# Kernel optimization log

Hardware: AMD Instinct MI355X
Metric: run time of the kernel (lower is better)

## Reference

```python
import jax, jax.numpy as jnp
import numpy as np

B, C, D = 512, 50000, 256
N_LOADED = 40000


def setup_inputs() -> dict:
    key = jax.random.key(0)
    k1, k2, k3, k4 = jax.random.split(key, 4)
    visual_feats = jax.random.normal(k1, (B, D), dtype=jnp.float32)
    text_feats = jax.random.normal(k2, (C, D), dtype=jnp.float32)
    # sparse multi-hot labels; force class 0 positive for every row so the
    # positive set (intersected with loaded ids) is never empty
    batch_label = (jax.random.uniform(k3, (B, C)) < 0.02).astype(jnp.int32)
    batch_label = batch_label.at[:, 0].set(1)
    # distinct loaded class ids; force id 0 to be loaded
    ids = jax.random.permutation(k4, C)[:N_LOADED].astype(jnp.int32)
    ids = jnp.sort(ids).at[0].set(0)
    return {
        "visual_feats": visual_feats,
        "text_feats": text_feats,
        "batch_label": batch_label,
        "class_ids_loaded": ids,
        "d_space": D,
    }


def reference(visual_feats, text_feats, batch_label, class_ids_loaded, d_space):
    num_classes = text_feats.shape[0]
    # membership mask for loaded class ids (the set() intersection in torch)
    loaded = jnp.zeros((num_classes,), dtype=bool).at[class_ids_loaded].set(True)

    # cosine similarity; note: torch adds 1e-6 eps only to text-feature norms
    v = visual_feats / jnp.linalg.norm(visual_feats, axis=1, keepdims=True)
    t = text_feats / (1e-6 + jnp.linalg.norm(text_feats, axis=1, keepdims=True))
    S = v @ t.T  # [B, C]

    pos = (batch_label != 0) & loaded[None, :]  # ragged positive sets, as mask
    neg = (batch_label == 0) & loaded[None, :]  # ragged negative sets, as mask

    # denominator: sum of exp(sim) over negatives, per row
    denom = jnp.sum(jnp.where(neg, jnp.exp(S), 0.0), axis=1)  # [B]
    n_pos = jnp.sum(pos, axis=1).astype(S.dtype)  # [B]

    # per-row loss: mean over positives of -log(exp(s_p)/denom) = log(denom)-s_p
    per_row = jnp.sum(jnp.where(pos, jnp.log(denom)[:, None] - S, 0.0), axis=1) / n_pos
    return jnp.mean(per_row).reshape(1)
```

## Files before the change

### kernel.cpp

```cpp
#include <hip/hip_runtime.h>
#include <math.h>

#define D_DIM 256
#define GTM 64
#define GTN 64
#define BK 32
#define NB 782
#define NBP 784

typedef __attribute__((ext_vector_type(8))) short short8;
typedef __attribute__((ext_vector_type(4))) float floatx4;
typedef unsigned long long u64;

__device__ __forceinline__ unsigned short f2bf(float f) {
    unsigned int u = __float_as_uint(f);
    u += 0x7FFFu + ((u >> 16) & 1u);
    return (unsigned short)(u >> 16);
}

__device__ __forceinline__ void gload16(const void* g, void* lds) {
    __builtin_amdgcn_global_load_lds(
        (const __attribute__((address_space(1))) unsigned int*)g,
        (__attribute__((address_space(3))) unsigned int*)lds, 16, 0, 0);
}

__global__ __launch_bounds__(256) void prep(
    const float* __restrict__ V, const float* __restrict__ T,
    const int* __restrict__ ids, u64* __restrict__ loadedmask,
    unsigned short* __restrict__ Vb, unsigned short* __restrict__ Tb,
    float* __restrict__ gaccum, unsigned int* __restrict__ gcount,
    int B, int C, int n_loaded, int WPR) {
    const int tid = threadIdx.x;
    const int lane = tid & 63;
    int ptid = blockIdx.x * 256 + tid;
    if (ptid == 0) { *gcount = 0u; *gaccum = 0.f; }
    if (ptid < WPR) {
        int base = ptid << 6;
        int lo = 0, hi = n_loaded;
        while (lo < hi) { int mid = (lo + hi) >> 1; if (ids[mid] < base) lo = mid + 1; else hi = mid; }
        u64 m = 0;
        for (int i = lo; i < n_loaded; ++i) {
            int v = ids[i]; if (v >= base + 64) break;
            m |= 1ull << (v - base);
        }
        loadedmask[ptid] = m;
    }
    int pwave = blockIdx.x * 4 + (tid >> 6);
    int r0 = pwave * 4;
    if (r0 >= B + C) return;
    float4 x[4];
    #pragma unroll
    for (int q = 0; q < 4; ++q) {
        int wv = r0 + q;
        if (wv < B + C) {
            const float* src = (wv < B) ? (V + (size_t)wv * D_DIM)
                                        : (T + (size_t)(wv - B) * D_DIM);
            x[q] = ((const float4*)src)[lane];
        }
    }
    #pragma unroll
    for (int q = 0; q < 4; ++q) {
        int wv = r0 + q;
        if (wv >= B + C) break;
        bool isV = wv < B;
        float ss = x[q].x * x[q].x + x[q].y * x[q].y + x[q].z * x[q].z + x[q].w * x[q].w;
        #pragma unroll
        for (int off = 32; off > 0; off >>= 1) ss += __shfl_xor(ss, off);
        float nrm = sqrtf(ss);
        float s = isV ? (1.0f / nrm) : (1.0f / (1e-6f + nrm));
        ushort4 o;
        o.x = f2bf(x[q].x * s); o.y = f2bf(x[q].y * s);
        o.z = f2bf(x[q].z * s); o.w = f2bf(x[q].w * s);
        unsigned short* dst = isV ? (Vb + (size_t)wv * D_DIM)
                                  : (Tb + (size_t)(wv - B) * D_DIM);
        ((ushort4*)dst)[lane] = o;
    }
}

__global__ __launch_bounds__(256) void gemm_fused(
    const unsigned short* __restrict__ Vb, const unsigned short* __restrict__ Tb,
    const int* __restrict__ label, const u64* __restrict__ loadedmask,
    float* __restrict__ denomP, float* __restrict__ posP, float* __restrict__ npP,
    int C, int WPR) {
    __shared__ unsigned short As[GTM * BK];
    __shared__ unsigned short Bs[GTN * BK];
    __shared__ u64 smask[GTM];
    __shared__ float sDen[GTM], sPos[GTM], sNp[GTM];

    const int tid  = threadIdx.x;
    const int lane = tid & 63;
    const int w    = tid >> 6;
    const int m0 = blockIdx.x * GTM;
    const int n0 = blockIdx.y * GTN;

    if (tid < GTM) { sDen[tid] = 0.f; sPos[tid] = 0.f; sNp[tid] = 0.f; }

    {
        int col = n0 + lane;
        if (col >= C) col = C - 1;
        const int* lp = label + (size_t)(m0 + w * 16) * C + col;
        int labv[16];
        #pragma unroll
        for (int i = 0; i < 16; ++i) labv[i] = lp[(size_t)i * C];
        #pragma unroll
        for (int i = 0; i < 16; ++i) {
            u64 bw = __ballot(labv[i] != 0);
            if (lane == 0) smask[w * 16 + i] = bw;
        }
    }

    const int sra = lane >> 2;
    const int kc  = (lane & 3) * 8;
    int ga = m0 + w * 16 + sra;
    int gb = n0 + w * 16 + sra;
    if (gb >= C) gb = C - 1;
    const unsigned short* gA = Vb + (size_t)ga * D_DIM + kc;
    const unsigned short* gB = Tb + (size_t)gb * D_DIM + kc;
    unsigned short* lA = &As[w * 16 * BK];
    unsigned short* lB = &Bs[w * 16 * BK];

    const int wm = (w >> 1) * 32;
    const int wn = (w & 1) * 32;
    const int fr = lane & 15;
    const int quad = lane >> 4;

    floatx4 acc[2][2];
    #pragma unroll
    for (int mi = 0; mi < 2; mi++)
        #pragma unroll
        for (int ni = 0; ni < 2; ni++) acc[mi][ni] = (floatx4)0.f;

    #pragma unroll
    for (int kt = 0; kt < D_DIM / BK; ++kt) {
        if (kt) __syncthreads();
        gload16(gA + kt * BK, lA);
        gload16(gB + kt * BK, lB);
        __syncthreads();
        short8 af[2], bf[2];
        #pragma unroll
        for (int mi = 0; mi < 2; mi++)
            af[mi] = *(const short8*)&As[(wm + mi * 16 + fr) * BK + quad * 8];
        #pragma unroll
        for (int ni = 0; ni < 2; ni++)
            bf[ni] = *(const short8*)&Bs[(wn + ni * 16 + fr) * BK + quad * 8];
        #pragma unroll
        for (int mi = 0; mi < 2; mi++)
            #pragma unroll
            for (int ni = 0; ni < 2; ni++)
                acc[mi][ni] = __builtin_amdgcn_mfma_f32_16x16x32_bf16(
                    af[mi], bf[ni], acc[mi][ni], 0, 0, 0);
    }

    const u64 loadedw = loadedmask[n0 >> 6];
    #pragma unroll
    for (int mi = 0; mi < 2; mi++) {
        #pragma unroll
        for (int i = 0; i < 4; i++) {
            const int mloc = wm + mi * 16 + quad * 4 + i;
            const u64 praw = smask[mloc];
            const u64 posw = praw & loadedw;
            const u64 negw = loadedw & ~praw;
            float den = 0.f, pos = 0.f, np = 0.f;
            #pragma unroll
            for (int ni = 0; ni < 2; ni++) {
                const float s = acc[mi][ni][i];
                const int bit = wn + ni * 16 + fr;
                if ((negw >> bit) & 1) den += __expf(s);
                if ((posw >> bit) & 1) { pos += s; np += 1.f; }
            }
            #pragma unroll
            for (int off = 8; off >= 1; off >>= 1) {
                den += __shfl_xor(den, off);
                pos += __shfl_xor(pos, off);
                np  += __shfl_xor(np, off);
            }
            if (fr == 0) {
                if (den != 0.f) atomicAdd(&sDen[mloc], den);
                if (np  != 0.f) { atomicAdd(&sPos[mloc], pos); atomicAdd(&sNp[mloc], np); }
            }
        }
    }
    __syncthreads();
    if (tid < GTM) {
        denomP[(size_t)(m0 + tid) * NBP + blockIdx.y] = sDen[tid];
        posP[(size_t)(m0 + tid) * NBP + blockIdx.y]   = sPos[tid];
        npP[(size_t)(m0 + tid) * NBP + blockIdx.y]    = sNp[tid];
    }
}

__global__ void reduce_rows(const float* __restrict__ denomP, const float* __restrict__ posP,
                            const float* __restrict__ npP,
                            float* __restrict__ gaccum, unsigned int* __restrict__ gcount,
                            float* __restrict__ out, int B) {
    __shared__ float bsum[4];
    int wv   = threadIdx.x >> 6;
    int row  = blockIdx.x * 4 + wv;
    int lane = threadIdx.x & 63;
    float den = 0.f, pos = 0.f, np = 0.f;
    if (row < B) {
        for (int bn = lane; bn < NB; bn += 64) {
            den += denomP[(size_t)row * NBP + bn];
            pos += posP[(size_t)row * NBP + bn];
            np  += npP[(size_t)row * NBP + bn];
        }
        #pragma unroll
        for (int off = 32; off > 0; off >>= 1) {
            den += __shfl_xor(den, off);
            pos += __shfl_xor(pos, off);
            np  += __shfl_xor(np, off);
        }
    }
    if (lane == 0) bsum[wv] = (row < B) ? (logf(den) - pos / np) : 0.f;
    __syncthreads();
    if (threadIdx.x == 0) {
        float s = bsum[0] + bsum[1] + bsum[2] + bsum[3];
        atomicAdd(gaccum, s);
        __threadfence();
        unsigned int old = atomicAdd(gcount, 1u);
        if (old == gridDim.x - 1) {
            float tot = atomicAdd(gaccum, 0.0f);
            out[0] = tot / (float)B;
        }
    }
}

extern "C" void kernel_launch(void* const* d_in, const int* in_sizes, int n_in,
                              void* d_out, int out_size, void* d_ws, size_t ws_size,
                              hipStream_t stream) {
    const float* V     = (const float*)d_in[0];
    const float* T     = (const float*)d_in[1];
    const int*   label = (const int*)d_in[2];
    const int*   ids   = (const int*)d_in[3];
    int B = in_sizes[0] / D_DIM;
    int C = in_sizes[1] / D_DIM;
    int n_loaded = in_sizes[3];
    int WPR = (C + 63) >> 6;

    char* ws = (char*)d_ws;
    float*        gaccum = (float*)(ws + 0);
    unsigned int* gcount = (unsigned int*)(ws + 8);
    u64*   loadedmask = (u64*)(ws + 2048);
    unsigned short* Vb = (unsigned short*)(ws + 8320);
    unsigned short* Tb = (unsigned short*)(ws + 270464);
    float* denomP  = (float*)(ws + 25870464);
    float* posP    = (float*)(ws + 27476096);
    float* npP     = (float*)(ws + 29081728);

    int prep_waves  = (B + C + 3) / 4;
    int prep_blocks = (prep_waves + 3) / 4;
    prep<<<prep_blocks, 256, 0, stream>>>(
        V, T, ids, loadedmask, Vb, Tb, gaccum, gcount, B, C, n_loaded, WPR);

    dim3 grid(B / GTM, NB);
    gemm_fused<<<grid, 256, 0, stream>>>(Vb, Tb, label, loadedmask,
                                         denomP, posP, npP, C, WPR);

    reduce_rows<<<(B + 3) / 4, 256, 0, stream>>>(denomP, posP, npP,
                                                 gaccum, gcount, (float*)d_out, B);
}
```

Before: 269.0 us.

## Fuse row normalization and bf16 conversion into GEMM, vectorize label mask load

Drops the separate prep pass that normalized and bf16-converted both feature matrices. The GEMM now loads raw fp32 tiles, converts them to bf16 in registers, stores them to LDS, accumulates sum-of-squares on the fly, and applies the inverse norms to each dot product in the epilogue. This removes a full read-write of the normalized copy, but every block now reads fp32 data, twice the bytes of bf16, and redundantly recomputes norms across the 8 M-blocks and 782 N-blocks. The label mask load also switches from 16 scalar strided loads plus a ballot per row to int4 vector loads combined with shuffles.

```diff
diff --git a/kernel.cpp b/kernel.cpp
--- a/kernel.cpp
+++ b/kernel.cpp
@@ -18,24 +18,22 @@
     return (unsigned short)(u >> 16);
 }
 
-__device__ __forceinline__ void gload16(const void* g, void* lds) {
-    __builtin_amdgcn_global_load_lds(
-        (const __attribute__((address_space(1))) unsigned int*)g,
-        (__attribute__((address_space(3))) unsigned int*)lds, 16, 0, 0);
-}
-
-__global__ __launch_bounds__(256) void prep(
-    const float* __restrict__ V, const float* __restrict__ T,
-    const int* __restrict__ ids, u64* __restrict__ loadedmask,
-    unsigned short* __restrict__ Vb, unsigned short* __restrict__ Tb,
-    float* __restrict__ gaccum, unsigned int* __restrict__ gcount,
-    int B, int C, int n_loaded, int WPR) {
-    const int tid = threadIdx.x;
-    const int lane = tid & 63;
-    int ptid = blockIdx.x * 256 + tid;
-    if (ptid == 0) { *gcount = 0u; *gaccum = 0.f; }
-    if (ptid < WPR) {
-        int base = ptid << 6;
+__device__ __forceinline__ short8 pack8(float4 x, float4 y) {
+    short8 r;
+    r[0] = (short)f2bf(x.x); r[1] = (short)f2bf(x.y);
+    r[2] = (short)f2bf(x.z); r[3] = (short)f2bf(x.w);
+    r[4] = (short)f2bf(y.x); r[5] = (short)f2bf(y.y);
+    r[6] = (short)f2bf(y.z); r[7] = (short)f2bf(y.w);
+    return r;
+}
+
+__global__ void prep_mask(const int* __restrict__ ids, u64* __restrict__ loadedmask,
+                          float* __restrict__ gaccum, unsigned int* __restrict__ gcount,
+                          int n_loaded, int WPR) {
+    int t = blockIdx.x * 256 + threadIdx.x;
+    if (t == 0) { *gcount = 0u; *gaccum = 0.f; }
+    if (t < WPR) {
+        int base = t << 6;
         int lo = 0, hi = n_loaded;
         while (lo < hi) { int mid = (lo + hi) >> 1; if (ids[mid] < base) lo = mid + 1; else hi = mid; }
         u64 m = 0;
@@ -43,48 +41,19 @@
             int v = ids[i]; if (v >= base + 64) break;
             m |= 1ull << (v - base);
         }
-        loadedmask[ptid] = m;
-    }
-    int pwave = blockIdx.x * 4 + (tid >> 6);
-    int r0 = pwave * 4;
-    if (r0 >= B + C) return;
-    float4 x[4];
-    #pragma unroll
-    for (int q = 0; q < 4; ++q) {
-        int wv = r0 + q;
-        if (wv < B + C) {
-            const float* src = (wv < B) ? (V + (size_t)wv * D_DIM)
-                                        : (T + (size_t)(wv - B) * D_DIM);
-            x[q] = ((const float4*)src)[lane];
-        }
-    }
-    #pragma unroll
-    for (int q = 0; q < 4; ++q) {
-        int wv = r0 + q;
-        if (wv >= B + C) break;
-        bool isV = wv < B;
-        float ss = x[q].x * x[q].x + x[q].y * x[q].y + x[q].z * x[q].z + x[q].w * x[q].w;
-        #pragma unroll
-        for (int off = 32; off > 0; off >>= 1) ss += __shfl_xor(ss, off);
-        float nrm = sqrtf(ss);
-        float s = isV ? (1.0f / nrm) : (1.0f / (1e-6f + nrm));
-        ushort4 o;
-        o.x = f2bf(x[q].x * s); o.y = f2bf(x[q].y * s);
-        o.z = f2bf(x[q].z * s); o.w = f2bf(x[q].w * s);
-        unsigned short* dst = isV ? (Vb + (size_t)wv * D_DIM)
-                                  : (Tb + (size_t)(wv - B) * D_DIM);
-        ((ushort4*)dst)[lane] = o;
+        loadedmask[t] = m;
     }
 }
 
 __global__ __launch_bounds__(256) void gemm_fused(
-    const unsigned short* __restrict__ Vb, const unsigned short* __restrict__ Tb,
+    const float* __restrict__ V, const float* __restrict__ T,
     const int* __restrict__ label, const u64* __restrict__ loadedmask,
     float* __restrict__ denomP, float* __restrict__ posP, float* __restrict__ npP,
     int C, int WPR) {
     __shared__ unsigned short As[GTM * BK];
     __shared__ unsigned short Bs[GTN * BK];
     __shared__ u64 smask[GTM];
+    __shared__ float sInvA[GTM], sInvB[GTN];
     __shared__ float sDen[GTM], sPos[GTM], sNp[GTM];
 
     const int tid  = threadIdx.x;
@@ -96,28 +65,38 @@
     if (tid < GTM) { sDen[tid] = 0.f; sPos[tid] = 0.f; sNp[tid] = 0.f; }
 
     {
-        int col = n0 + lane;
-        if (col >= C) col = C - 1;
-        const int* lp = label + (size_t)(m0 + w * 16) * C + col;
-        int labv[16];
-        #pragma unroll
-        for (int i = 0; i < 16; ++i) labv[i] = lp[(size_t)i * C];
-        #pragma unroll
-        for (int i = 0; i < 16; ++i) {
-            u64 bw = __ballot(labv[i] != 0);
-            if (lane == 0) smask[w * 16 + i] = bw;
+        const int cg = (lane & 15) * 4;
+        int colbase = n0 + cg;
+        if (colbase > C - 4) colbase = C - 4;
+        int4 q[4];
+        #pragma unroll
+        for (int p = 0; p < 4; ++p) {
+            int r = m0 + w * 16 + (lane >> 4) + p * 4;
+            q[p] = *(const int4*)(label + (size_t)r * C + colbase);
+        }
+        #pragma unroll
+        for (int p = 0; p < 4; ++p) {
+            unsigned int nib = (q[p].x ? 1u : 0u) | (q[p].y ? 2u : 0u) |
+                               (q[p].z ? 4u : 0u) | (q[p].w ? 8u : 0u);
+            u64 wv = (u64)nib << cg;
+            wv |= __shfl_xor(wv, 1);
+            wv |= __shfl_xor(wv, 2);
+            wv |= __shfl_xor(wv, 4);
+            wv |= __shfl_xor(wv, 8);
+            if ((lane & 15) == 0) smask[w * 16 + (lane >> 4) + p * 4] = wv;
         }
     }
 
     const int sra = lane >> 2;
-    const int kc  = (lane & 3) * 8;
+    const int kq  = lane & 3;
+    const int kc  = kq * 8;
     int ga = m0 + w * 16 + sra;
     int gb = n0 + w * 16 + sra;
     if (gb >= C) gb = C - 1;
-    const unsigned short* gA = Vb + (size_t)ga * D_DIM + kc;
-    const unsigned short* gB = Tb + (size_t)gb * D_DIM + kc;
-    unsigned short* lA = &As[w * 16 * BK];
-    unsigned short* lB = &Bs[w * 16 * BK];
+    const float* gA = V + (size_t)ga * D_DIM + kc;
+    const float* gB = T + (size_t)gb * D_DIM + kc;
+    unsigned short* lA = &As[(w * 16 + sra) * BK + kc];
+    unsigned short* lB = &Bs[(w * 16 + sra) * BK + kc];
 
     const int wm = (w >> 1) * 32;
     const int wn = (w & 1) * 32;
@@ -130,11 +109,21 @@
         #pragma unroll
         for (int ni = 0; ni < 2; ni++) acc[mi][ni] = (floatx4)0.f;
 
+    float ssA = 0.f, ssB = 0.f;
+
     #pragma unroll
     for (int kt = 0; kt < D_DIM / BK; ++kt) {
+        float4 a0 = *(const float4*)(gA + kt * BK);
+        float4 a1 = *(const float4*)(gA + kt * BK + 4);
+        float4 b0 = *(const float4*)(gB + kt * BK);
+        float4 b1 = *(const float4*)(gB + kt * BK + 4);
         if (kt) __syncthreads();
-        gload16(gA + kt * BK, lA);
-        gload16(gB + kt * BK, lB);
+        ssA += a0.x*a0.x + a0.y*a0.y + a0.z*a0.z + a0.w*a0.w
+             + a1.x*a1.x + a1.y*a1.y + a1.z*a1.z + a1.w*a1.w;
+        ssB += b0.x*b0.x + b0.y*b0.y + b0.z*b0.z + b0.w*b0.w
+             + b1.x*b1.x + b1.y*b1.y + b1.z*b1.z + b1.w*b1.w;
+        *(short8*)lA = pack8(a0, a1);
+        *(short8*)lB = pack8(b0, b1);
         __syncthreads();
         short8 af[2], bf[2];
         #pragma unroll
@@ -151,22 +140,31 @@
                     af[mi], bf[ni], acc[mi][ni], 0, 0, 0);
     }
 
+    ssA += __shfl_xor(ssA, 1); ssA += __shfl_xor(ssA, 2);
+    ssB += __shfl_xor(ssB, 1); ssB += __shfl_xor(ssB, 2);
+    if (kq == 0) {
+        sInvA[w * 16 + sra] = 1.0f / sqrtf(ssA);
+        sInvB[w * 16 + sra] = 1.0f / (1e-6f + sqrtf(ssB));
+    }
+    __syncthreads();
+
     const u64 loadedw = loadedmask[n0 >> 6];
     #pragma unroll
     for (int mi = 0; mi < 2; mi++) {
         #pragma unroll
         for (int i = 0; i < 4; i++) {
             const int mloc = wm + mi * 16 + quad * 4 + i;
+            const float invA = sInvA[mloc];
             const u64 praw = smask[mloc];
             const u64 posw = praw & loadedw;
             const u64 negw = loadedw & ~praw;
             float den = 0.f, pos = 0.f, np = 0.f;
             #pragma unroll
             for (int ni = 0; ni < 2; ni++) {
-                const float s = acc[mi][ni][i];
-                const int bit = wn + ni * 16 + fr;
-                if ((negw >> bit) & 1) den += __expf(s);
-                if ((posw >> bit) & 1) { pos += s; np += 1.f; }
+                const int nloc = wn + ni * 16 + fr;
+                const float s = acc[mi][ni][i] * invA * sInvB[nloc];
+                if ((negw >> nloc) & 1) den += __expf(s);
+                if ((posw >> nloc) & 1) { pos += s; np += 1.f; }
             }
             #pragma unroll
             for (int off = 8; off >= 1; off >>= 1) {
@@ -240,19 +238,15 @@
     float*        gaccum = (float*)(ws + 0);
     unsigned int* gcount = (unsigned int*)(ws + 8);
     u64*   loadedmask = (u64*)(ws + 2048);
-    unsigned short* Vb = (unsigned short*)(ws + 8320);
-    unsigned short* Tb = (unsigned short*)(ws + 270464);
-    float* denomP  = (float*)(ws + 25870464);
-    float* posP    = (float*)(ws + 27476096);
-    float* npP     = (float*)(ws + 29081728);
-
-    int prep_waves  = (B + C + 3) / 4;
-    int prep_blocks = (prep_waves + 3) / 4;
-    prep<<<prep_blocks, 256, 0, stream>>>(
-        V, T, ids, loadedmask, Vb, Tb, gaccum, gcount, B, C, n_loaded, WPR);
+    float* denomP  = (float*)(ws + 8320);
+    float* posP    = (float*)(ws + 1613952);
+    float* npP     = (float*)(ws + 3219584);
+
+    prep_mask<<<(WPR + 255) / 256, 256, 0, stream>>>(
+        ids, loadedmask, gaccum, gcount, n_loaded, WPR);
 
     dim3 grid(B / GTM, NB);
-    gemm_fused<<<grid, 256, 0, stream>>>(Vb, Tb, label, loadedmask,
+    gemm_fused<<<grid, 256, 0, stream>>>(V, T, label, loadedmask,
                                          denomP, posP, npP, C, WPR);
 
     reduce_rows<<<(B + 3) / 4, 256, 0, stream>>>(denomP, posP, npP,
```

Result: slower. 296.6 us (+10.3%).
